# Kernel tuning notes

Hardware: AMD Instinct MI355X
Metric: run time of the kernel (lower is better)

The kernel has to match this reference:

```python
import jax, jax.numpy as jnp
import numpy as np

N1 = 10000; N2 = 10000; F_IN = 128; HID = 128; H = 8; D = HID // H; L = 2
E12 = 320000; E21 = 320000; EF = 500000


def setup_inputs() -> dict:
    key = jax.random.key(0)
    keys = jax.random.split(key, 64)
    ctr = [0]
    def nk():
        k = keys[ctr[0]]; ctr[0] += 1; return k
    def rn(shape, s=0.05):
        return jax.random.normal(nk(), shape, jnp.float32) * s
    inp = {
        'x_n1': rn((N1, F_IN), 1.0),
        'x_n2': rn((N2, F_IN), 1.0),
        'W_in1': rn((F_IN, HID)), 'b_in1': jnp.zeros((HID,), jnp.float32),
        'W_in2': rn((F_IN, HID)), 'b_in2': jnp.zeros((HID,), jnp.float32),
    }
    for t in ('n1', 'n2'):
        for p in ('k', 'q', 'v', 'a'):
            inp['W%s_%s' % (p, t)] = rn((L, HID, HID))
            inp['b%s_%s' % (p, t)] = jnp.zeros((L, HID), jnp.float32)
        inp['skip_%s' % t] = jnp.ones((L,), jnp.float32)
    for r in ('12', '21'):
        inp['a_rel_%s' % r] = rn((L, H, D, D), 0.1)
        inp['m_rel_%s' % r] = rn((L, H, D, D), 0.1)
        inp['p_rel_%s' % r] = jnp.ones((L, H), jnp.float32)
    inp['ei_12'] = jax.random.randint(nk(), (2, E12), 0, N2)  # row0: src in n1, row1: dst in n2
    inp['ei_21'] = jax.random.randint(nk(), (2, E21), 0, N1)  # row0: src in n2, row1: dst in n1
    inp['edge_index'] = jax.random.randint(nk(), (2, EF), 0, N1)  # (m_index, d_index) query pairs
    return inp


def _seg_softmax(alpha, seg, n):
    # numerically-stable softmax over incoming edges per destination node
    m = jax.ops.segment_max(alpha, seg, num_segments=n)
    e = jnp.exp(alpha - m[seg])
    s = jax.ops.segment_sum(e, seg, num_segments=n)
    return e / (s[seg] + 1e-16)


def _het_attn(k_src, v_src, q_dst, src, dst, a_rel, m_rel, p_rel, n_dst):
    # HGTConv per-edge-type attention: relation-specific K/V transform,
    # dot-product attention with prior p_rel, segment softmax, scatter-add.
    ke = jnp.einsum('nhd,hde->nhe', k_src, a_rel)   # [Ns,H,D]
    ve = jnp.einsum('nhd,hde->nhe', v_src, m_rel)   # [Ns,H,D]
    alpha = jnp.einsum('ehd,ehd->eh', q_dst[dst], ke[src]) * p_rel / jnp.sqrt(jnp.float32(D))
    w = _seg_softmax(alpha, dst, n_dst)             # [E,H]
    return jax.ops.segment_sum(w[..., None] * ve[src], dst, num_segments=n_dst)  # [Nd,H,D]


def reference(x_n1, x_n2, W_in1, b_in1, W_in2, b_in2,
              Wk_n1, bk_n1, Wq_n1, bq_n1, Wv_n1, bv_n1, Wa_n1, ba_n1, skip_n1,
              Wk_n2, bk_n2, Wq_n2, bq_n2, Wv_n2, bv_n2, Wa_n2, ba_n2, skip_n2,
              a_rel_12, m_rel_12, p_rel_12, a_rel_21, m_rel_21, p_rel_21,
              ei_12, ei_21, edge_index):
    # per-type input projection + relu
    x1 = jax.nn.relu(x_n1 @ W_in1 + b_in1)
    x2 = jax.nn.relu(x_n2 @ W_in2 + b_in2)
    s12, d12 = ei_12[0], ei_12[1]
    s21, d21 = ei_21[0], ei_21[1]
    outs1, outs2 = [], []
    for l in range(L):
        k1 = (x1 @ Wk_n1[l] + bk_n1[l]).reshape(N1, H, D)
        q1 = (x1 @ Wq_n1[l] + bq_n1[l]).reshape(N1, H, D)
        v1 = (x1 @ Wv_n1[l] + bv_n1[l]).reshape(N1, H, D)
        k2 = (x2 @ Wk_n2[l] + bk_n2[l]).reshape(N2, H, D)
        q2 = (x2 @ Wq_n2[l] + bq_n2[l]).reshape(N2, H, D)
        v2 = (x2 @ Wv_n2[l] + bv_n2[l]).reshape(N2, H, D)
        agg2 = _het_attn(k1, v1, q2, s12, d12, a_rel_12[l], m_rel_12[l], p_rel_12[l], N2)
        agg1 = _het_attn(k2, v2, q1, s21, d21, a_rel_21[l], m_rel_21[l], p_rel_21[l], N1)
        o1 = jax.nn.gelu(agg1.reshape(N1, HID), approximate=False) @ Wa_n1[l] + ba_n1[l]
        o2 = jax.nn.gelu(agg2.reshape(N2, HID), approximate=False) @ Wa_n2[l] + ba_n2[l]
        b1 = jax.nn.sigmoid(skip_n1[l]); x1 = b1 * o1 + (1.0 - b1) * x1
        b2 = jax.nn.sigmoid(skip_n2[l]); x2 = b2 * o2 + (1.0 - b2) * x2
        outs1.append(x1); outs2.append(x2)
    Em = jnp.concatenate(outs1, axis=1)  # [N1, HID*L]
    Ed = jnp.concatenate(outs2, axis=1)  # [N2, HID*L]
    # (Em @ Ed.T)[m,d] computed as a sparse gather-dot (same math, no N1xN2 matrix)
    y = jnp.einsum('ec,ec->e', Em[edge_index[0]], Ed[edge_index[1]])[:, None]
    return y
```

## Files before the change

### kernel.cpp

```cpp
#include <hip/hip_runtime.h>
#include <cstdint>
#include <cstddef>

typedef unsigned short ushort_t;
typedef __attribute__((ext_vector_type(8))) short bf16x8;
typedef __attribute__((ext_vector_type(4))) float f32x4;

#define PN1   10000
#define PN2   10000
#define NH    8
#define NLAY  2
#define NE12  320000
#define NE21  320000
#define NEF   500000
#define DL    10016
#define NBIN  8
#define BINW  1250
#define BCF   65536
#define DOTK  1024
#define NB2   20
#define BC2   20480

__device__ __forceinline__ unsigned f2bf(float f) {
  union { float f; unsigned u; } v; v.f = f;
  return (v.u + 0x7FFFu + ((v.u >> 16) & 1u)) >> 16;
}
__device__ __forceinline__ float bf2f(unsigned s) {
  union { float f; unsigned u; } v; v.u = s << 16; return v.f;
}
union U4 { uint4 u; bf16x8 s; };

__device__ __forceinline__ float dpp_red8(float x) {
  int t;
  t = __builtin_amdgcn_update_dpp(0, __float_as_int(x), 0xB1,  0xf, 0xf, true);
  x += __int_as_float(t);
  t = __builtin_amdgcn_update_dpp(0, __float_as_int(x), 0x4E,  0xf, 0xf, true);
  x += __int_as_float(t);
  t = __builtin_amdgcn_update_dpp(0, __float_as_int(x), 0x141, 0xf, 0xf, true);
  x += __int_as_float(t);
  return x;
}
__device__ __forceinline__ float dpp_red4(float x) {
  int t;
  t = __builtin_amdgcn_update_dpp(0, __float_as_int(x), 0xB1, 0xf, 0xf, true);
  x += __int_as_float(t);
  t = __builtin_amdgcn_update_dpp(0, __float_as_int(x), 0x4E, 0xf, 0xf, true);
  x += __int_as_float(t);
  return x;
}
__device__ __forceinline__ float dpp_xor1(float x) {
  return __int_as_float(__builtin_amdgcn_update_dpp(0, __float_as_int(x), 0xB1, 0xf, 0xf, true));
}

#define GB 157

__device__ __forceinline__ void stage_A(const float* __restrict__ X, unsigned* sA,
                                        int rowbase, int N, int tid)
{
#pragma unroll
  for (int i = 0; i < 8; ++i) {
    int idx = tid + i * 256;
    int r = idx >> 5;
    int c4 = (idx & 31) << 2;
    int gr = rowbase + r;
    float4 v = make_float4(0.f, 0.f, 0.f, 0.f);
    if (gr < N) v = *(const float4*)(X + (size_t)gr * 128 + c4);
    sA[r * 68 + (c4 >> 1)]     = f2bf(v.x) | (f2bf(v.y) << 16);
    sA[r * 68 + (c4 >> 1) + 1] = f2bf(v.z) | (f2bf(v.w) << 16);
  }
}

__device__ __forceinline__ void stage_B(const unsigned* __restrict__ Wt, unsigned* sB, int tid)
{
#pragma unroll
  for (int i = 0; i < 8; ++i) {
    int idx = tid + i * 256;
    int n = idx >> 4;
    int k4 = (idx & 15) << 2;
    *(uint4*)&sB[n * 68 + k4] = *(const uint4*)&Wt[(size_t)idx << 2];
  }
}

__device__ __forceinline__ void mfma_compute(const unsigned* sA, const unsigned* sB,
                                             int w, int lane, f32x4 acc[8])
{
#pragma unroll
  for (int ks = 0; ks < 4; ++ks) {
    U4 a; a.u = *(const uint4*)&sA[(w * 16 + (lane & 15)) * 68 + ks * 16 + ((lane >> 4) << 2)];
#pragma unroll
    for (int t = 0; t < 8; ++t) {
      U4 b; b.u = *(const uint4*)&sB[(t * 16 + (lane & 15)) * 68 + ks * 16 + ((lane >> 4) << 2)];
      acc[t] = __builtin_amdgcn_mfma_f32_16x16x32_bf16(a.s, b.s, acc[t], 0, 0, 0);
    }
  }
}

__launch_bounds__(256, 2)
__global__ void mfma_gemm1(const float* __restrict__ X1, const float* __restrict__ X2,
                           const unsigned* __restrict__ W1t, const float* __restrict__ b1,
                           const unsigned* __restrict__ W2t, const float* __restrict__ b2,
                           float* __restrict__ Y1, float* __restrict__ Y2,
                           int nb1, int N, int mode,
                           const float* __restrict__ skip1, const float* __restrict__ skip2,
                           ushort_t* __restrict__ cat1, ushort_t* __restrict__ cat2, int catoff)
{
  __shared__ unsigned sA[64 * 68];
  __shared__ unsigned sB[128 * 68];
  const int tid = threadIdx.x;
  const bool t2 = blockIdx.x >= nb1;
  const int rowbase = (t2 ? blockIdx.x - nb1 : blockIdx.x) * 64;
  const float* X = t2 ? X2 : X1;
  const unsigned* Wt = t2 ? W2t : W1t;
  const float* bias = t2 ? b2 : b1;
  float* Y = t2 ? Y2 : Y1;
  ushort_t* cat = t2 ? cat2 : cat1;

  stage_A(X, sA, rowbase, N, tid);
  stage_B(Wt, sB, tid);
  __syncthreads();

  const int w = tid >> 6, lane = tid & 63;
  f32x4 acc[8];
#pragma unroll
  for (int t = 0; t < 8; ++t) acc[t] = (f32x4){0.f, 0.f, 0.f, 0.f};
  mfma_compute(sA, sB, w, lane, acc);

  float beta = 0.f;
  if (mode >= 2) beta = 1.0f / (1.0f + expf(-((t2 ? skip2 : skip1)[0])));
  const int cb = lane & 15;
  const int rq = (lane >> 4) << 2;
#pragma unroll
  for (int t = 0; t < 8; ++t) {
    int c = t * 16 + cb;
    float bv = bias[c];
#pragma unroll
    for (int r = 0; r < 4; ++r) {
      int row = rowbase + w * 16 + rq + r;
      float val = acc[t][r] + bv;
      if (mode == 0) {
        if (row < N) Y[(size_t)row * 128 + c] = fmaxf(val, 0.f);
      } else {
        float xo = (row < N) ? Y[(size_t)row * 128 + c] : 0.f;
        float tv = beta * val + (1.f - beta) * xo;
        if (mode == 2 && row < N) Y[(size_t)row * 128 + c] = tv;
        float nb = dpp_xor1(tv);
        if (((lane & 1) == 0) && row < N)
          *(unsigned*)(cat + (size_t)row * 256 + catoff + c) = f2bf(tv) | (f2bf(nb) << 16);
      }
    }
  }
}

__launch_bounds__(256, 2)
__global__ void mfma_gemm_kvq(const float* __restrict__ A1, const float* __restrict__ A2,
                              const unsigned* __restrict__ W0T1, const float* __restrict__ b0_1,
                              const unsigned* __restrict__ W0T2, const float* __restrict__ b0_2,
                              float* __restrict__ Y1, float* __restrict__ Y2,
                              int nb1, int N, int mode,
                              const float* __restrict__ skip1, const float* __restrict__ skip2,
                              ushort_t* __restrict__ cat1, ushort_t* __restrict__ cat2, int catoff,
                              const unsigned* __restrict__ WqT1, const unsigned* __restrict__ WkT1,
                              const unsigned* __restrict__ WvT1,
                              const float* __restrict__ bq1, const float* __restrict__ bk1,
                              const float* __restrict__ bv1,
                              const unsigned* __restrict__ WqT2, const unsigned* __restrict__ WkT2,
                              const unsigned* __restrict__ WvT2,
                              const float* __restrict__ bq2, const float* __restrict__ bk2,
                              const float* __restrict__ bv2,
                              float* __restrict__ q1o, unsigned* __restrict__ kv1,
                              float* __restrict__ q2o, unsigned* __restrict__ kv2)
{
  __shared__ unsigned sA[64 * 68];
  __shared__ unsigned sB[128 * 68];
  const int tid = threadIdx.x;
  const bool t2 = blockIdx.x >= nb1;
  const int rowbase = (t2 ? blockIdx.x - nb1 : blockIdx.x) * 64;
  const float* A = t2 ? A2 : A1;
  const unsigned* W0 = t2 ? W0T2 : W0T1;
  const float* bias0 = t2 ? b0_2 : b0_1;
  float* Y = t2 ? Y2 : Y1;
  ushort_t* cat = t2 ? cat2 : cat1;

  stage_A(A, sA, rowbase, N, tid);
  stage_B(W0, sB, tid);
  __syncthreads();

  const int w = tid >> 6, lane = tid & 63;
  const int cb = lane & 15;
  const int rq = (lane >> 4) << 2;

  f32x4 acc[8];
#pragma unroll
  for (int t = 0; t < 8; ++t) acc[t] = (f32x4){0.f, 0.f, 0.f, 0.f};
  mfma_compute(sA, sB, w, lane, acc);

  float beta = 0.f;
  if (mode == 2) beta = 1.0f / (1.0f + expf(-((t2 ? skip2 : skip1)[0])));

#pragma unroll
  for (int t = 0; t < 8; ++t) {
    int c = t * 16 + cb;
    float bv = bias0[c];
#pragma unroll
    for (int r = 0; r < 4; ++r) {
      int row = rowbase + w * 16 + rq + r;
      float val = acc[t][r] + bv;
      if (mode == 0) {
        val = fmaxf(val, 0.f);
        if (row < N) Y[(size_t)row * 128 + c] = val;
      } else {
        float xo = (row < N) ? Y[(size_t)row * 128 + c] : 0.f;
        val = beta * val + (1.f - beta) * xo;
        if (row < N) Y[(size_t)row * 128 + c] = val;
        float nb = dpp_xor1(val);
        if (((lane & 1) == 0) && row < N)
          *(unsigned*)(cat + (size_t)row * 256 + catoff + c) = f2bf(val) | (f2bf(nb) << 16);
      }
      acc[t][r] = val;
    }
  }

  __syncthreads();
#pragma unroll
  for (int t = 0; t < 8; ++t) {
#pragma unroll
    for (int r = 0; r < 4; ++r) {
      float nb = dpp_xor1(acc[t][r]);
      if ((lane & 1) == 0)
        sA[(w * 16 + rq + r) * 68 + ((t * 16 + cb) >> 1)] = f2bf(acc[t][r]) | (f2bf(nb) << 16);
    }
  }

  const unsigned* Wt[3] = { t2 ? WqT2 : WqT1, t2 ? WkT2 : WkT1, t2 ? WvT2 : WvT1 };
  const float* bs[3] = { t2 ? bq2 : bq1, t2 ? bk2 : bk1, t2 ? bv2 : bv1 };
  float* qo = t2 ? q2o : q1o;
  unsigned* kvo = t2 ? kv2 : kv1;

  for (int j = 0; j < 3; ++j) {
    __syncthreads();
    stage_B(Wt[j], sB, tid);
    __syncthreads();
#pragma unroll
    for (int t = 0; t < 8; ++t) acc[t] = (f32x4){0.f, 0.f, 0.f, 0.f};
    mfma_compute(sA, sB, w, lane, acc);

#pragma unroll
    for (int t = 0; t < 8; ++t) {
      int c = t * 16 + cb;
      float bv = bs[j][c];
#pragma unroll
      for (int r = 0; r < 4; ++r) {
        int row = rowbase + w * 16 + rq + r;
        float val = acc[t][r] + bv;
        if (j == 0) {
          if (row < N) qo[(size_t)row * 128 + c] = val;
        } else {
          float nb = dpp_xor1(val);
          if (((lane & 1) == 0) && row < N) {
            unsigned pk = f2bf(val) | (f2bf(nb) << 16);
            kvo[(size_t)row * 128 + c + (j == 1 ? 0 : 1)] = pk;
          }
        }
      }
    }
  }
}

__global__ void prep(const float* W_in1, const float* W_in2,
                     const float* Wq_n1, const float* Wq_n2,
                     const float* Wa_n1, const float* Wa_n2,
                     const float* Wk_n1, const float* bk_n1,
                     const float* Wv_n1, const float* bv_n1,
                     const float* Wk_n2, const float* bk_n2,
                     const float* Wv_n2, const float* bv_n2,
                     const float* a_rel_12, const float* m_rel_12,
                     const float* a_rel_21, const float* m_rel_21,
                     unsigned* WinT1, unsigned* WinT2,
                     unsigned* WqT1, unsigned* WqT2,
                     unsigned* WaT1, unsigned* WaT2,
                     unsigned* WkT1, float* bkF1, unsigned* WvT1, float* bvF1,
                     unsigned* WkT2, float* bkF2, unsigned* WvT2, float* bvF2,
                     int* zc)
{
  const int yid = blockIdx.y;
  int idx = blockIdx.x * 256 + threadIdx.x;

  if (yid < 10) {
    if (idx >= 8192) return;
    const float* W; unsigned* Wt;
    switch (yid) {
      case 0: W = W_in1;          Wt = WinT1;        break;
      case 1: W = W_in2;          Wt = WinT2;        break;
      case 2: W = Wq_n1;          Wt = WqT1;         break;
      case 3: W = Wq_n1 + 16384;  Wt = WqT1 + 8192;  break;
      case 4: W = Wq_n2;          Wt = WqT2;         break;
      case 5: W = Wq_n2 + 16384;  Wt = WqT2 + 8192;  break;
      case 6: W = Wa_n1;          Wt = WaT1;         break;
      case 7: W = Wa_n1 + 16384;  Wt = WaT1 + 8192;  break;
      case 8: W = Wa_n2;          Wt = WaT2;         break;
      default: W = Wa_n2 + 16384; Wt = WaT2 + 8192;  break;
    }
    int n = idx & 127, kp = idx >> 7;
    float a = W[(size_t)(2 * kp) * 128 + n];
    float b = W[(size_t)(2 * kp + 1) * 128 + n];
    Wt[n * 64 + kp] = f2bf(a) | (f2bf(b) << 16);
  } else if (yid < 18) {
    int job = yid - 10;
    int l = job >> 2, m = job & 3;
    const float *W, *b, *rel; unsigned* Wt; float* bf;
    switch (m) {
      case 0:  W = Wk_n1; b = bk_n1; rel = a_rel_12; Wt = WkT1; bf = bkF1; break;
      case 1:  W = Wv_n1; b = bv_n1; rel = m_rel_12; Wt = WvT1; bf = bvF1; break;
      case 2:  W = Wk_n2; b = bk_n2; rel = a_rel_21; Wt = WkT2; bf = bkF2; break;
      default: W = Wv_n2; b = bv_n2; rel = m_rel_21; Wt = WvT2; bf = bvF2; break;
    }
    W += (size_t)l * 16384; b += l * 128; rel += (size_t)l * 2048;
    Wt += (size_t)l * 8192; bf += l * 128;
    if (idx < 8192) {
      int n = idx & 127, kp = idx >> 7;
      int h = n >> 4, e = n & 15;
      const float* rr = rel + h * 256;
      const float* s0 = W + (size_t)(2 * kp) * 128 + h * 16;
      const float* s1 = s0 + 128;
      float a0 = 0.f, a1 = 0.f;
#pragma unroll
      for (int d = 0; d < 16; ++d) {
        float rv = rr[d * 16 + e];
        a0 = fmaf(s0[d], rv, a0);
        a1 = fmaf(s1[d], rv, a1);
      }
      Wt[n * 64 + kp] = f2bf(a0) | (f2bf(a1) << 16);
    } else if (idx < 8320) {
      int n = idx - 8192;
      int h = n >> 4, e = n & 15;
      const float* rr = rel + h * 256;
      float a = 0.f;
#pragma unroll
      for (int d = 0; d < 16; ++d) a = fmaf(b[h * 16 + d], rr[d * 16 + e], a);
      bf[n] = a;
    }
  } else {
    if (idx < 64) zc[idx] = 0;
  }
}

__launch_bounds__(1024)
__global__ void partition_all(const int* __restrict__ ei12, const int* __restrict__ ei21,
                              const int* __restrict__ eif,
                              int* __restrict__ cnt12, int* __restrict__ pay12,
                              int* __restrict__ cnt21, int* __restrict__ pay21,
                              int* __restrict__ cntF, int2* __restrict__ payF)
{
  __shared__ int cnt[NB2], base[NB2];
  const int t = threadIdx.x;
  const int job = blockIdx.y;
  if (job < 2) {
    const int* ei = job ? ei21 : ei12;
    int* gcnt = job ? cnt21 : cnt12;
    int* pay  = job ? pay21 : pay12;
    if (t < NB2) cnt[t] = 0;
    __syncthreads();
    int e = blockIdx.x * 1024 + t;
    const bool v = e < NE12;
    int b = 0, off = 0, w = 0;
    if (v) {
      int s = ei[e], d = ei[NE12 + e];
      b = d >> 9;
      w = ((d & 511) << 14) | s;
      off = atomicAdd(&cnt[b], 1);
    }
    __syncthreads();
    if (t < NB2) base[t] = cnt[t] ? atomicAdd(&gcnt[t], cnt[t]) : 0;
    __syncthreads();
    if (v) pay[b * BC2 + base[b] + off] = w;
  } else {
    if (t < NBIN) cnt[t] = 0;
    __syncthreads();
    int e = blockIdx.x * 1024 + t;
    const bool v = e < NEF;
    int b = 0, off = 0, m = 0, d = 0;
    if (v) {
      m = eif[e]; d = eif[NEF + e];
      b = m / BINW;
      off = atomicAdd(&cnt[b], 1);
    }
    __syncthreads();
    if (t < NBIN) base[t] = cnt[t] ? atomicAdd(&cntF[t], cnt[t]) : 0;
    __syncthreads();
    if (v) { int2 w2; w2.x = (m << 16) | d; w2.y = e; payF[(size_t)b * BCF + base[b] + off] = w2; }
  }
}

__launch_bounds__(1024)
__global__ void binsort(const int* __restrict__ cnt12, const int* __restrict__ pay12,
                        int* __restrict__ rowptr12, int* __restrict__ csr12,
                        const int* __restrict__ cnt21, const int* __restrict__ pay21,
                        int* __restrict__ rowptr21, int* __restrict__ csr21)
{
  const int wg = blockIdx.x;
  const int g = wg / NB2, b = wg % NB2;
  const int* gcnt = g ? cnt21 : cnt12;
  const int* pay  = (g ? pay21 : pay12) + (size_t)b * BC2;
  int* rowptr = g ? rowptr21 : rowptr12;
  int* csr    = g ? csr21 : csr12;
  const int t = threadIdx.x;
  const int n = gcnt[b];
  int gbase = 0;
#pragma unroll
  for (int i = 0; i < NB2; ++i) gbase += (i < b) ? gcnt[i] : 0;

  __shared__ int hist[512];
  __shared__ int wsum[8];
  if (t < 512) hist[t] = 0;
  __syncthreads();
  for (int i = t; i < n; i += 1024)
    atomicAdd(&hist[pay[i] >> 14], 1);
  __syncthreads();
  int hv = (t < 512) ? hist[t] : 0;
  int inc = hv;
#pragma unroll
  for (int off = 1; off < 64; off <<= 1) {
    int v = __shfl_up(inc, off);
    if ((t & 63) >= off) inc += v;
  }
  if (t < 512 && (t & 63) == 63) wsum[t >> 6] = inc;
  __syncthreads();
  if (t == 0) {
    int run = 0;
#pragma unroll
    for (int i = 0; i < 8; ++i) { int v = wsum[i]; wsum[i] = run; run += v; }
  }
  __syncthreads();
  int pre = (t < 512) ? (wsum[t >> 6] + inc - hv) : 0;
  __syncthreads();
  if (t < 512) hist[t] = pre;
  int node = b * 512 + t;
  if (t < 512 && node < PN1) rowptr[node] = gbase + pre;
  if (b == NB2 - 1 && t == 0) rowptr[PN1] = gbase + n;
  __syncthreads();
  for (int i = t; i < n; i += 1024) {
    int w = pay[i];
    int p = atomicAdd(&hist[w >> 14], 1);
    csr[gbase + p] = w & 16383;
  }
}

__launch_bounds__(256)
__global__ void edge_dot_part(const int* __restrict__ cntF, const int2* __restrict__ payF,
                              const ushort_t* __restrict__ Em, const ushort_t* __restrict__ Ed,
                              float* __restrict__ y)
{
  const int part = blockIdx.x & 7;
  const int chunk = blockIdx.x >> 3;
  const int lo = part * BCF;
  const int hi = lo + cntF[part];
  const int t = threadIdx.x;
  const int g = t >> 3, gl = t & 7;

  for (int i0 = lo + chunk * 64; i0 < hi; i0 += DOTK * 64) {
    int s0 = i0 + 2 * g;
    int s1 = s0 + 1;
    const bool h0 = s0 < hi, h1 = s1 < hi;
    int2 w0 = h0 ? payF[s0] : make_int2(0, 0);
    int2 w1 = h1 ? payF[s1] : w0;
    int m0 = w0.x >> 16, d0 = w0.x & 0xffff;
    int m1 = w1.x >> 16, d1 = w1.x & 0xffff;

    const uint4* A0 = (const uint4*)(Em + (size_t)m0 * 256);
    const uint4* B0 = (const uint4*)(Ed + (size_t)d0 * 256);
    const uint4* A1 = (const uint4*)(Em + (size_t)m1 * 256);
    const uint4* B1 = (const uint4*)(Ed + (size_t)d1 * 256);

    uint4 a0[4], b0[4], a1[4], b1[4];
#pragma unroll
    for (int i = 0; i < 4; ++i) { a0[i] = A0[gl + 8 * i]; b0[i] = B0[gl + 8 * i]; }
#pragma unroll
    for (int i = 0; i < 4; ++i) { a1[i] = A1[gl + 8 * i]; b1[i] = B1[gl + 8 * i]; }

    float acc0 = 0.f, acc1 = 0.f;
#pragma unroll
    for (int i = 0; i < 4; ++i) {
      uint4 a = a0[i], b = b0[i];
      acc0 = fmaf(bf2f(a.x & 0xffffu), bf2f(b.x & 0xffffu), acc0);
      acc0 = fmaf(bf2f(a.x >> 16),     bf2f(b.x >> 16),     acc0);
      acc0 = fmaf(bf2f(a.y & 0xffffu), bf2f(b.y & 0xffffu), acc0);
      acc0 = fmaf(bf2f(a.y >> 16),     bf2f(b.y >> 16),     acc0);
      acc0 = fmaf(bf2f(a.z & 0xffffu), bf2f(b.z & 0xffffu), acc0);
      acc0 = fmaf(bf2f(a.z >> 16),     bf2f(b.z >> 16),     acc0);
      acc0 = fmaf(bf2f(a.w & 0xffffu), bf2f(b.w & 0xffffu), acc0);
      acc0 = fmaf(bf2f(a.w >> 16),     bf2f(b.w >> 16),     acc0);
    }
#pragma unroll
    for (int i = 0; i < 4; ++i) {
      uint4 a = a1[i], b = b1[i];
      acc1 = fmaf(bf2f(a.x & 0xffffu), bf2f(b.x & 0xffffu), acc1);
      acc1 = fmaf(bf2f(a.x >> 16),     bf2f(b.x >> 16),     acc1);
      acc1 = fmaf(bf2f(a.y & 0xffffu), bf2f(b.y & 0xffffu), acc1);
      acc1 = fmaf(bf2f(a.y >> 16),     bf2f(b.y >> 16),     acc1);
      acc1 = fmaf(bf2f(a.z & 0xffffu), bf2f(b.z & 0xffffu), acc1);
      acc1 = fmaf(bf2f(a.z >> 16),     bf2f(b.z >> 16),     acc1);
      acc1 = fmaf(bf2f(a.w & 0xffffu), bf2f(b.w & 0xffffu), acc1);
      acc1 = fmaf(bf2f(a.w >> 16),     bf2f(b.w >> 16),     acc1);
    }
    acc0 = dpp_red8(acc0);
    acc1 = dpp_red8(acc1);
    if (gl == 0) {
      if (h0) y[w0.y] = acc0;
      if (h1) y[w1.y] = acc1;
    }
  }
}

__launch_bounds__(256)
__global__ void attn_gather2(const int* __restrict__ rowptr12, const int* __restrict__ csr12,
                             const float* __restrict__ q2, const unsigned* __restrict__ kv1,
                             const float* __restrict__ pr12,
                             const int* __restrict__ rowptr21, const int* __restrict__ csr21,
                             const float* __restrict__ q1, const unsigned* __restrict__ kv2,
                             const float* __restrict__ pr21,
                             float* __restrict__ agg2, float* __restrict__ agg1)
{
  const int wid = (blockIdx.x * 256 + threadIdx.x) >> 6;
  const int lane = threadIdx.x & 63;
  const int sub = lane >> 5;
  const int sl = lane & 31;
  const bool dirB = wid >= PN2;
  const int d = __builtin_amdgcn_readfirstlane(dirB ? wid - PN2 : wid);
  const int* rowptr = dirB ? rowptr21 : rowptr12;
  const int* csr    = dirB ? csr21 : csr12;
  const float* q    = dirB ? q1 : q2;
  const unsigned* kv = dirB ? kv2 : kv1;
  const float* prel = dirB ? pr21 : pr12;
  float* agg = dirB ? agg1 : agg2;

  const int h = sl >> 2;
  const float4 qv = *(const float4*)(q + (size_t)d * 128 + 4 * sl);
  const float pr2 = prel[h] * (0.25f * 1.4426950408889634f);
  const int beg = __builtin_amdgcn_readfirstlane(rowptr[d]);
  const int end = __builtin_amdgcn_readfirstlane(rowptr[d + 1]);
  const int co = 4 * sl;

  float ssum = 0.f, a0 = 0.f, a1 = 0.f, a2 = 0.f, a3 = 0.f;

  uint4 buf[4];
#pragma unroll
  for (int j = 0; j < 4; ++j) {
    int idx = beg + 2 * j + sub;
    int s = (idx < end) ? csr[idx] : 0;
    buf[j] = *(const uint4*)(kv + (size_t)s * 128 + co);
  }

  for (int i = beg; i < end; i += 8) {
    uint4 cur[4];
#pragma unroll
    for (int j = 0; j < 4; ++j) cur[j] = buf[j];
#pragma unroll
    for (int j = 0; j < 4; ++j) {
      int idx = i + 8 + 2 * j + sub;
      int s = (idx < end) ? csr[idx] : 0;
      buf[j] = *(const uint4*)(kv + (size_t)s * 128 + co);
    }
    float p[4], ex[4];
#pragma unroll
    for (int j = 0; j < 4; ++j) {
      float t = qv.x * bf2f(cur[j].x & 0xffffu);
      t = fmaf(qv.y, bf2f(cur[j].x >> 16), t);
      t = fmaf(qv.z, bf2f(cur[j].z & 0xffffu), t);
      p[j] = fmaf(qv.w, bf2f(cur[j].z >> 16), t);
    }
#pragma unroll
    for (int j = 0; j < 4; ++j) p[j] = dpp_red4(p[j]);
#pragma unroll
    for (int j = 0; j < 4; ++j)
      ex[j] = (i + 2 * j + sub < end) ? exp2f(p[j] * pr2) : 0.f;
    ssum += (ex[0] + ex[1]) + (ex[2] + ex[3]);
#pragma unroll
    for (int j = 0; j < 4; ++j) {
      a0 = fmaf(ex[j], bf2f(cur[j].y & 0xffffu), a0);
      a1 = fmaf(ex[j], bf2f(cur[j].y >> 16),     a1);
      a2 = fmaf(ex[j], bf2f(cur[j].w & 0xffffu), a2);
      a3 = fmaf(ex[j], bf2f(cur[j].w >> 16),     a3);
    }
  }

  ssum += __shfl_xor(ssum, 32);
  a0 += __shfl_xor(a0, 32);
  a1 += __shfl_xor(a1, 32);
  a2 += __shfl_xor(a2, 32);
  a3 += __shfl_xor(a3, 32);

  if (sub == 0) {
    const float inv = 1.0f / (ssum + 1e-16f);
    float o0 = a0 * inv, o1 = a1 * inv, o2 = a2 * inv, o3 = a3 * inv;
    o0 = 0.5f * o0 * (1.f + erff(o0 * 0.70710678118654752f));
    o1 = 0.5f * o1 * (1.f + erff(o1 * 0.70710678118654752f));
    o2 = 0.5f * o2 * (1.f + erff(o2 * 0.70710678118654752f));
    o3 = 0.5f * o3 * (1.f + erff(o3 * 0.70710678118654752f));
    float4 out; out.x = o0; out.y = o1; out.z = o2; out.w = o3;
    *(float4*)(agg + (size_t)d * 128 + co) = out;
  }
}

extern "C" void kernel_launch(void* const* d_in, const int* in_sizes, int n_in,
                              void* d_out, int out_size, void* d_ws, size_t ws_size,
                              hipStream_t stream)
{
  const float* x_n1  = (const float*)d_in[0];
  const float* x_n2  = (const float*)d_in[1];
  const float* W_in1 = (const float*)d_in[2];
  const float* b_in1 = (const float*)d_in[3];
  const float* W_in2 = (const float*)d_in[4];
  const float* b_in2 = (const float*)d_in[5];
  const float* Wk_n1 = (const float*)d_in[6];
  const float* bk_n1 = (const float*)d_in[7];
  const float* Wq_n1 = (const float*)d_in[8];
  const float* bq_n1 = (const float*)d_in[9];
  const float* Wv_n1 = (const float*)d_in[10];
  const float* bv_n1 = (const float*)d_in[11];
  const float* Wa_n1 = (const float*)d_in[12];
  const float* ba_n1 = (const float*)d_in[13];
  const float* skip_n1 = (const float*)d_in[14];
  const float* Wk_n2 = (const float*)d_in[15];
  const float* bk_n2 = (const float*)d_in[16];
  const float* Wq_n2 = (const float*)d_in[17];
  const float* bq_n2 = (const float*)d_in[18];
  const float* Wv_n2 = (const float*)d_in[19];
  const float* bv_n2 = (const float*)d_in[20];
  const float* Wa_n2 = (const float*)d_in[21];
  const float* ba_n2 = (const float*)d_in[22];
  const float* skip_n2 = (const float*)d_in[23];
  const float* a_rel_12 = (const float*)d_in[24];
  const float* m_rel_12 = (const float*)d_in[25];
  const float* p_rel_12 = (const float*)d_in[26];
  const float* a_rel_21 = (const float*)d_in[27];
  const float* m_rel_21 = (const float*)d_in[28];
  const float* p_rel_21 = (const float*)d_in[29];
  const int*   ei_12 = (const int*)d_in[30];
  const int*   ei_21 = (const int*)d_in[31];
  const int*   edge_index = (const int*)d_in[32];
  float* y = (float*)d_out;

  const size_t NF = (size_t)PN1 * 128;
  float* ws = (float*)d_ws;
  float* x1   = ws + 0 * NF;
  float* x2   = ws + 1 * NF;
  float* q1   = ws + 2 * NF;
  float* q2   = ws + 3 * NF;
  float* agg1 = ws + 4 * NF;
  float* agg2 = ws + 5 * NF;
  unsigned* kv1 = (unsigned*)(ws + 6 * NF);
  unsigned* kv2 = (unsigned*)(ws + 7 * NF);
  ushort_t* Em  = (ushort_t*)(ws + 8 * NF);
  ushort_t* Ed  = (ushort_t*)(ws + 8 * NF + 1280000);
  unsigned* wb = (unsigned*)(ws + 8 * NF + 2560000);
  unsigned* WkT1 = wb;                     float* bkF1 = (float*)(wb + 16384);
  unsigned* WvT1 = wb + 16640;             float* bvF1 = (float*)(wb + 33024);
  unsigned* WkT2 = wb + 33280;             float* bkF2 = (float*)(wb + 49664);
  unsigned* WvT2 = wb + 49920;             float* bvF2 = (float*)(wb + 66304);
  unsigned* WinT1 = wb + 66560;
  unsigned* WinT2 = wb + 74752;
  unsigned* WqT1  = wb + 82944;
  unsigned* WqT2  = wb + 99328;
  unsigned* WaT1  = wb + 115712;
  unsigned* WaT2  = wb + 132096;
  int* ip = (int*)(wb + 148480);
  int* rowptr12 = ip;
  int* rowptr21 = ip + DL;
  int* zc       = ip + 2 * DL;
  int* cnt12 = zc;
  int* cnt21 = zc + 20;
  int* cntF  = zc + 40;
  int* csr12 = ip + 2 * DL + 64;
  int* csr21 = csr12 + NE12;
  int* pay12 = csr21 + NE21;
  int* pay21 = pay12 + NB2 * BC2;
  int2* payF = (int2*)(pay21 + NB2 * BC2);

  prep<<<dim3(33, 19), 256, 0, stream>>>(
      W_in1, W_in2, Wq_n1, Wq_n2, Wa_n1, Wa_n2,
      Wk_n1, bk_n1, Wv_n1, bv_n1, Wk_n2, bk_n2, Wv_n2, bv_n2,
      a_rel_12, m_rel_12, a_rel_21, m_rel_21,
      WinT1, WinT2, WqT1, WqT2, WaT1, WaT2,
      WkT1, bkF1, WvT1, bvF1, WkT2, bkF2, WvT2, bvF2, zc);

  const int PAB = (NEF + 1023) / 1024;
  partition_all<<<dim3(PAB, 3), 1024, 0, stream>>>(
      ei_12, ei_21, edge_index,
      cnt12, pay12, cnt21, pay21, cntF, payF);
  binsort<<<2 * NB2, 1024, 0, stream>>>(
      cnt12, pay12, rowptr12, csr12,
      cnt21, pay21, rowptr21, csr21);

  mfma_gemm_kvq<<<2 * GB, 256, 0, stream>>>(
      x_n1, x_n2, WinT1, b_in1, WinT2, b_in2,
      x1, x2, GB, PN1, 0, nullptr, nullptr, nullptr, nullptr, 0,
      WqT1, WkT1, WvT1, bq_n1, bkF1, bvF1,
      WqT2, WkT2, WvT2, bq_n2, bkF2, bvF2,
      q1, kv1, q2, kv2);

  attn_gather2<<<(2 * PN1) / 4, 256, 0, stream>>>(
      rowptr12, csr12, q2, kv1, p_rel_12,
      rowptr21, csr21, q1, kv2, p_rel_21,
      agg2, agg1);

  mfma_gemm_kvq<<<2 * GB, 256, 0, stream>>>(
      agg1, agg2, WaT1, ba_n1, WaT2, ba_n2,
      x1, x2, GB, PN1, 2, skip_n1, skip_n2, Em, Ed, 0,
      WqT1 + 8192, WkT1 + 8192, WvT1 + 8192, bq_n1 + 128, bkF1 + 128, bvF1 + 128,
      WqT2 + 8192, WkT2 + 8192, WvT2 + 8192, bq_n2 + 128, bkF2 + 128, bvF2 + 128,
      q1, kv1, q2, kv2);

  attn_gather2<<<(2 * PN1) / 4, 256, 0, stream>>>(
      rowptr12, csr12, q2, kv1, p_rel_12 + NH,
      rowptr21, csr21, q1, kv2, p_rel_21 + NH,
      agg2, agg1);

  mfma_gemm1<<<2 * GB, 256, 0, stream>>>(
      agg1, agg2, WaT1 + 8192, ba_n1 + 128, WaT2 + 8192, ba_n2 + 128,
      x1, x2, GB, PN1, 3, skip_n1 + 1, skip_n2 + 1, Em, Ed, 128);

  edge_dot_part<<<NBIN * DOTK, 256, 0, stream>>>(cntF, payF, Em, Ed, y);
}
```

Before: 337.8 us.

## Sub-sort CSR neighbors and final query pairs by source for locality

Binsort now builds a finer histogram keyed by destination node and by 512-wide source sub-range, so each node's CSR neighbor list is grouped by source index. A new dsort kernel counting-sorts each query-pair partition by d-index bucket into a second payload buffer. The edge-dot kernel reads that sorted buffer and runs a grid-stride loop with 256 chunks per partition instead of 1024. The aim is better cache reuse of gathered Em/Ed and K/V rows. The cost is an extra kernel launch with a serial 80-bucket prefix scan, plus a larger shared histogram in binsort.

```diff
diff --git a/kernel.cpp b/kernel.cpp
--- a/kernel.cpp
+++ b/kernel.cpp
@@ -17,9 +17,10 @@
 #define NBIN  8
 #define BINW  1250
 #define BCF   65536
-#define DOTK  1024
+#define DCH   256
 #define NB2   20
 #define BC2   20480
+#define SRB   20
 
 __device__ __forceinline__ unsigned f2bf(float f) {
   union { float f; unsigned u; } v; v.f = f;
@@ -409,44 +410,80 @@
 #pragma unroll
   for (int i = 0; i < NB2; ++i) gbase += (i < b) ? gcnt[i] : 0;
 
-  __shared__ int hist[512];
-  __shared__ int wsum[8];
-  if (t < 512) hist[t] = 0;
-  __syncthreads();
-  for (int i = t; i < n; i += 1024)
-    atomicAdd(&hist[pay[i] >> 14], 1);
-  __syncthreads();
-  int hv = (t < 512) ? hist[t] : 0;
-  int inc = hv;
+  __shared__ int hist[512 * SRB];
+  __shared__ int wsum[16];
+#pragma unroll
+  for (int i = 0; i < 10; ++i) hist[t + i * 1024] = 0;
+  __syncthreads();
+  for (int i = t; i < n; i += 1024) {
+    int w = pay[i];
+    atomicAdd(&hist[(w >> 14) * SRB + ((w & 16383) >> 9)], 1);
+  }
+  __syncthreads();
+  int cv[10];
+  int s = 0;
+#pragma unroll
+  for (int i = 0; i < 10; ++i) { cv[i] = hist[t * 10 + i]; s += cv[i]; }
+  int inc = s;
 #pragma unroll
   for (int off = 1; off < 64; off <<= 1) {
     int v = __shfl_up(inc, off);
     if ((t & 63) >= off) inc += v;
   }
-  if (t < 512 && (t & 63) == 63) wsum[t >> 6] = inc;
+  if ((t & 63) == 63) wsum[t >> 6] = inc;
   __syncthreads();
   if (t == 0) {
     int run = 0;
 #pragma unroll
-    for (int i = 0; i < 8; ++i) { int v = wsum[i]; wsum[i] = run; run += v; }
-  }
-  __syncthreads();
-  int pre = (t < 512) ? (wsum[t >> 6] + inc - hv) : 0;
-  __syncthreads();
-  if (t < 512) hist[t] = pre;
-  int node = b * 512 + t;
-  if (t < 512 && node < PN1) rowptr[node] = gbase + pre;
+    for (int i = 0; i < 16; ++i) { int v = wsum[i]; wsum[i] = run; run += v; }
+  }
+  __syncthreads();
+  int run = wsum[t >> 6] + (inc - s);
+#pragma unroll
+  for (int i = 0; i < 10; ++i) { hist[t * 10 + i] = run; run += cv[i]; }
+  __syncthreads();
+  if (t < 512) {
+    int node = b * 512 + t;
+    if (node < PN1) rowptr[node] = gbase + hist[t * SRB];
+  }
   if (b == NB2 - 1 && t == 0) rowptr[PN1] = gbase + n;
   __syncthreads();
   for (int i = t; i < n; i += 1024) {
     int w = pay[i];
-    int p = atomicAdd(&hist[w >> 14], 1);
+    int p = atomicAdd(&hist[(w >> 14) * SRB + ((w & 16383) >> 9)], 1);
     csr[gbase + p] = w & 16383;
   }
 }
 
+__launch_bounds__(1024)
+__global__ void dsort(const int* __restrict__ cntF, const int2* __restrict__ payF,
+                      int2* __restrict__ payF2)
+{
+  const int part = blockIdx.x;
+  const int n = cntF[part];
+  const int2* src = payF + (size_t)part * BCF;
+  int2* dst = payF2 + (size_t)part * BCF;
+  __shared__ int hist[80];
+  const int t = threadIdx.x;
+  if (t < 80) hist[t] = 0;
+  __syncthreads();
+  for (int i = t; i < n; i += 1024)
+    atomicAdd(&hist[(src[i].x & 0xffff) >> 7], 1);
+  __syncthreads();
+  if (t == 0) {
+    int run = 0;
+    for (int i = 0; i < 80; ++i) { int v = hist[i]; hist[i] = run; run += v; }
+  }
+  __syncthreads();
+  for (int i = t; i < n; i += 1024) {
+    int2 w = src[i];
+    int p = atomicAdd(&hist[(w.x & 0xffff) >> 7], 1);
+    dst[p] = w;
+  }
+}
+
 __launch_bounds__(256)
-__global__ void edge_dot_part(const int* __restrict__ cntF, const int2* __restrict__ payF,
+__global__ void edge_dot_part(const int* __restrict__ cntF, const int2* __restrict__ payF2,
                               const ushort_t* __restrict__ Em, const ushort_t* __restrict__ Ed,
                               float* __restrict__ y)
 {
@@ -457,12 +494,14 @@
   const int t = threadIdx.x;
   const int g = t >> 3, gl = t & 7;
 
-  for (int i0 = lo + chunk * 64; i0 < hi; i0 += DOTK * 64) {
+  for (int k = 0;; ++k) {
+    int i0 = lo + (chunk + k * DCH) * 64;
+    if (i0 >= hi) break;
     int s0 = i0 + 2 * g;
     int s1 = s0 + 1;
     const bool h0 = s0 < hi, h1 = s1 < hi;
-    int2 w0 = h0 ? payF[s0] : make_int2(0, 0);
-    int2 w1 = h1 ? payF[s1] : w0;
+    int2 w0 = h0 ? payF2[s0] : make_int2(0, 0);
+    int2 w1 = h1 ? payF2[s1] : w0;
     int m0 = w0.x >> 16, d0 = w0.x & 0xffff;
     int m1 = w1.x >> 16, d1 = w1.x & 0xffff;
 
@@ -674,7 +713,8 @@
   int* csr21 = csr12 + NE12;
   int* pay12 = csr21 + NE21;
   int* pay21 = pay12 + NB2 * BC2;
-  int2* payF = (int2*)(pay21 + NB2 * BC2);
+  int2* payF  = (int2*)(pay21 + NB2 * BC2);
+  int2* payF2 = payF + (size_t)NBIN * BCF;
 
   prep<<<dim3(33, 19), 256, 0, stream>>>(
       W_in1, W_in2, Wq_n1, Wq_n2, Wa_n1, Wa_n2,
@@ -690,6 +730,7 @@
   binsort<<<2 * NB2, 1024, 0, stream>>>(
       cnt12, pay12, rowptr12, csr12,
       cnt21, pay21, rowptr21, csr21);
+  dsort<<<NBIN, 1024, 0, stream>>>(cntF, payF, payF2);
 
   mfma_gemm_kvq<<<2 * GB, 256, 0, stream>>>(
       x_n1, x_n2, WinT1, b_in1, WinT2, b_in2,
@@ -719,5 +760,5 @@
       agg1, agg2, WaT1 + 8192, ba_n1 + 128, WaT2 + 8192, ba_n2 + 128,
       x1, x2, GB, PN1, 3, skip_n1 + 1, skip_n2 + 1, Em, Ed, 128);
 
-  edge_dot_part<<<NBIN * DOTK, 256, 0, stream>>>(cntF, payF, Em, Ed, y);
-}
+  edge_dot_part<<<NBIN * DCH, 256, 0, stream>>>(cntF, payF2, Em, Ed, y);
+}
```

Measured after the change: 380.9 us. 12.8% more time.
